# Kernel optimization log

Hardware: AMD Instinct MI355X
Metric: run time of the kernel (lower is better)

## Reference

```python
import jax, jax.numpy as jnp
import numpy as np
from jax import lax

BIG = 1e10  # initial distance, matching torch's 1e10


def farthest_point_sample(xyz, init_farthest, npoint):
    """xyz: [B,N,3] float; init_farthest: [B] int32; returns centroids [B,npoint] int32."""
    B, N, _ = xyz.shape
    batch_idx = jnp.arange(B)

    def body(i, state):
        centroids, distance, farthest = state
        centroids = centroids.at[:, i].set(farthest)
        c = xyz[batch_idx, farthest][:, None, :]              # [B,1,3] current centroid
        dist = jnp.sum(jnp.square(xyz - c), axis=-1)          # [B,N] sq. distance
        distance = jnp.minimum(distance, dist)                # mask-update: keep min dist to any centroid
        farthest = jnp.argmax(distance, axis=-1).astype(jnp.int32)
        return centroids, distance, farthest

    centroids0 = jnp.zeros((B, npoint), jnp.int32)
    distance0 = jnp.full((B, N), BIG, xyz.dtype)
    centroids, _, _ = lax.fori_loop(0, npoint, body, (centroids0, distance0, init_farthest.astype(jnp.int32)))
    return centroids


def setup_inputs() -> dict:
    key = jax.random.key(0)
    k1, k2, k3 = jax.random.split(key, 3)
    B, N = 16, 100000
    mesh = jax.random.normal(k1, (B, N, 3), dtype=jnp.float32)
    contact_map = jax.random.uniform(k2, (B, N, 1), dtype=jnp.float32)
    init_farthest = jax.random.randint(k3, (B,), 0, N, dtype=jnp.int32)
    return {"mesh": mesh, "contact_map": contact_map, "init_farthest": init_farthest, "npoint": 1024}


def reference(mesh, contact_map, init_farthest, npoint):
    B, N, _ = mesh.shape
    batch_idx = jnp.arange(B)

    # __compute_mesh_scale: max distance from centroid, per batch
    centroid = jnp.mean(mesh, axis=1, keepdims=True)                      # [B,1,3]
    s_obj = jnp.max(jnp.sqrt(jnp.sum(jnp.square(mesh - centroid), axis=2)), axis=1)  # [B]

    # __farthest_point_sample
    centroids = farthest_point_sample(mesh, init_farthest, npoint)        # [B,npoint]

    # gather sampled points and contact values
    point_cloud = mesh[batch_idx[:, None], centroids]                     # [B,npoint,3]
    cm_sampled = contact_map[batch_idx[:, None], centroids]               # [B,npoint,1]

    # normalize by object scale (broadcast over points/coords)
    point_cloud_norm = point_cloud / s_obj[:, None, None]

    # point_cloud_norm_contact fed to the contact encoder in the original
    return jnp.concatenate([cm_sampled, point_cloud_norm], axis=2)        # [B,npoint,4]
```

## Files before the change

kernel.cpp:

```cpp
#include <hip/hip_runtime.h>
#include <cstdint>

#define NBATCH 16
#define NPOINT 1024
#define NPTS   100000
#define GPB    16
#define TPB    256
#define WPB    4
#define NSUB   16
#define STRIDE (GPB * TPB)
#define KPT    25
#define NPAIR  13

typedef unsigned long long u64;
typedef unsigned int u32;


__global__ __launch_bounds__(256) void sum_kernel(const float* __restrict__ xyz,
                                                  float* __restrict__ psum) {
    const int b   = blockIdx.x & 15;
    const int sub = blockIdx.x >> 4;
    const float* P = xyz + (size_t)b * NPTS * 3;
    float sx = 0.f, sy = 0.f, sz = 0.f;
    for (int i = sub * TPB + threadIdx.x; i < NPTS; i += NSUB * TPB) {
        sx += P[i * 3 + 0];
        sy += P[i * 3 + 1];
        sz += P[i * 3 + 2];
    }
    #pragma unroll
    for (int off = 32; off; off >>= 1) {
        sx += __shfl_xor(sx, off);
        sy += __shfl_xor(sy, off);
        sz += __shfl_xor(sz, off);
    }
    __shared__ float r[3][4];
    const int wave = threadIdx.x >> 6, lane = threadIdx.x & 63;
    if (lane == 0) { r[0][wave] = sx; r[1][wave] = sy; r[2][wave] = sz; }
    __syncthreads();
    if (threadIdx.x == 0) {
        float* o = psum + (b * NSUB + sub) * 4;
        o[0] = r[0][0] + r[0][1] + r[0][2] + r[0][3];
        o[1] = r[1][0] + r[1][1] + r[1][2] + r[1][3];
        o[2] = r[2][0] + r[2][1] + r[2][2] + r[2][3];
    }
}

__global__ __launch_bounds__(256) void max_kernel(const float* __restrict__ xyz,
                                                  const float* __restrict__ psum,
                                                  unsigned* __restrict__ pmax,
                                                  u64* __restrict__ slots) {
    if (blockIdx.x == 0) {
        slots[threadIdx.x] = 0ull;
        slots[threadIdx.x + 256] = 0ull;
    }
    const int b   = blockIdx.x & 15;
    const int sub = blockIdx.x >> 4;
    const float* P = xyz + (size_t)b * NPTS * 3;
    float sx = 0.f, sy = 0.f, sz = 0.f;
    #pragma unroll
    for (int s = 0; s < NSUB; ++s) {
        sx += psum[(b * NSUB + s) * 4 + 0];
        sy += psum[(b * NSUB + s) * 4 + 1];
        sz += psum[(b * NSUB + s) * 4 + 2];
    }
    const float mx = sx / (float)NPTS, my = sy / (float)NPTS, mz = sz / (float)NPTS;
    float best = 0.f;
    for (int i = sub * TPB + threadIdx.x; i < NPTS; i += NSUB * TPB) {
        float dx = P[i * 3 + 0] - mx;
        float dy = P[i * 3 + 1] - my;
        float dz = P[i * 3 + 2] - mz;
        best = fmaxf(best, dx * dx + dy * dy + dz * dz);
    }
    #pragma unroll
    for (int off = 32; off; off >>= 1) best = fmaxf(best, __shfl_xor(best, off));
    __shared__ float r[4];
    const int wave = threadIdx.x >> 6, lane = threadIdx.x & 63;
    if (lane == 0) r[wave] = best;
    __syncthreads();
    if (threadIdx.x == 0)
        pmax[b * NSUB + sub] = __float_as_uint(fmaxf(fmaxf(r[0], r[1]), fmaxf(r[2], r[3])));
}

__device__ __forceinline__ u64 wave_max_u64(u64 k) {
    u32 lo = (u32)k, hi = (u32)(k >> 32);
    #define DPP_STEP(CTRL) do {                                                          \
        u32 olo = (u32)__builtin_amdgcn_update_dpp((int)lo, (int)lo, CTRL, 0xf, 0xf, false); \
        u32 ohi = (u32)__builtin_amdgcn_update_dpp((int)hi, (int)hi, CTRL, 0xf, 0xf, false); \
        u64 oo = ((u64)ohi << 32) | olo;                                                 \
        u64 cc = ((u64)hi  << 32) | lo;                                                  \
        if (oo > cc) { lo = olo; hi = ohi; }                                             \
    } while (0)
    DPP_STEP(0x111);
    DPP_STEP(0x112);
    DPP_STEP(0x114);
    DPP_STEP(0x118);
    DPP_STEP(0x142);
    DPP_STEP(0x143);
    #undef DPP_STEP
    return ((u64)hi << 32) | lo;
}

__device__ __forceinline__ u64 bcast_lane63(u64 v) {
    u32 lo = (u32)__builtin_amdgcn_readlane((int)(u32)v, 63);
    u32 hi = (u32)__builtin_amdgcn_readlane((int)(u32)(v >> 32), 63);
    return ((u64)hi << 32) | lo;
}

__device__ __forceinline__ void store_agent(u64* p, u64 v) {
    __hip_atomic_store(p, v, __ATOMIC_RELAXED, __HIP_MEMORY_SCOPE_AGENT);
}
__device__ __forceinline__ u64 load_agent(u64* p) {
    return __hip_atomic_load(p, __ATOMIC_RELAXED, __HIP_MEMORY_SCOPE_AGENT);
}

__global__ void
__attribute__((amdgpu_flat_work_group_size(256, 256), amdgpu_waves_per_eu(1, 1)))
fps_kernel(const float* __restrict__ xyz,
           const float* __restrict__ cmap,
           const int* __restrict__ init_far,
           const unsigned* __restrict__ pmax,
           u64* __restrict__ slots,
           float* __restrict__ out) {
    const int b   = blockIdx.x & 15;
    const int g   = blockIdx.x >> 4;
    const int tid = threadIdx.x;
    const int wave = tid >> 6, lane = tid & 63;
    const int tl  = g * TPB + tid;
    const float* P = xyz + (size_t)b * NPTS * 3;

    float m0 = 0.f;
    #pragma unroll
    for (int s = 0; s < NSUB; ++s) m0 = fmaxf(m0, __uint_as_float(pmax[b * NSUB + s]));
    const float sb = sqrtf(m0);

    float pxx[NPAIR], pxy[NPAIR], pyx[NPAIR], pyy[NPAIR],
          pzx[NPAIR], pzy[NPAIR], pdx[NPAIR], pdy[NPAIR];
    #pragma unroll
    for (int j = 0; j < NPAIR; ++j) {
        const int p0 = tl + (2 * j) * STRIDE;
        const int p1 = tl + (2 * j + 1) * STRIDE;
        const bool v0 = p0 < NPTS, v1 = p1 < NPTS;
        pxx[j] = v0 ? P[p0 * 3 + 0] : 0.f;  pxy[j] = v1 ? P[p1 * 3 + 0] : 0.f;
        pyx[j] = v0 ? P[p0 * 3 + 1] : 0.f;  pyy[j] = v1 ? P[p1 * 3 + 1] : 0.f;
        pzx[j] = v0 ? P[p0 * 3 + 2] : 0.f;  pzy[j] = v1 ? P[p1 * 3 + 2] : 0.f;
        pdx[j] = v0 ? 1e10f : -1.0f;        pdy[j] = v1 ? 1e10f : -1.0f;
    }

    __shared__ u64 lkey[WPB];
    __shared__ u64 pub;
    __shared__ int curhist[NPOINT];
    if (tid == 0) pub = 0;
    if (tid < WPB) lkey[tid] = 0;
    __syncthreads();

    int cur = init_far[b];
    float cx = P[cur * 3 + 0], cy = P[cur * 3 + 1], cz = P[cur * 3 + 2];

    for (int i = 0; i < NPOINT; ++i) {
        if (tid == 192) curhist[i] = cur;
        if (i == NPOINT - 1) break;

        float best = -1.0f;
        int bidx = 0;
        {
            #pragma clang fp contract(off)
            #pragma unroll
            for (int j = 0; j < NPAIR; ++j) {
                float dx0 = pxx[j] - cx, dx1 = pxy[j] - cx;
                float dy0 = pyx[j] - cy, dy1 = pyy[j] - cy;
                float dz0 = pzx[j] - cz, dz1 = pzy[j] - cz;
                float s0 = dx0 * dx0 + dy0 * dy0;  float s1 = dx1 * dx1 + dy1 * dy1;
                s0 = s0 + dz0 * dz0;               s1 = s1 + dz1 * dz1;
                float n0 = fminf(pdx[j], s0);      float n1 = fminf(pdy[j], s1);
                pdx[j] = n0;                       pdy[j] = n1;
                if (n0 > best) { best = n0; bidx = tl + (2 * j) * STRIDE; }
                if (n1 > best) { best = n1; bidx = tl + (2 * j + 1) * STRIDE; }
            }
        }

        const u64 want = (u64)(i + 1);
        u64 key = ((u64)__float_as_uint(best) << 22) | (u64)(0x3FFFFFu - (unsigned)bidx);
        const u64 wkey = wave_max_u64(key) | (want << 54);
        if (lane == 63)
            __hip_atomic_store(&lkey[wave], wkey, __ATOMIC_RELAXED,
                               __HIP_MEMORY_SCOPE_WORKGROUP);

        u64* const bs = slots + ((size_t)(i & 1) * NBATCH + b) * GPB;

        if (wave == 0) {
            u64 k;
            for (;;) {
                k = (lane < WPB)
                    ? __hip_atomic_load(&lkey[lane], __ATOMIC_RELAXED,
                                        __HIP_MEMORY_SCOPE_WORKGROUP)
                    : (want << 54);
                if (__all((int)((k >> 54) >= want))) break;
            }
            const u64 bk = wave_max_u64(lane < WPB ? k : 0);
            if (lane == 63) store_agent(&bs[g], bk);

            u64 v;
            {
                u64* sp = &bs[lane & 15];
                u64 vcur = load_agent(sp);
                u64 vnxt = load_agent(sp);
                int tries = 0;
                for (;;) {
                    if (__all((int)((vcur >> 54) >= want))) { v = vcur; break; }
                    vcur = vnxt;
                    vnxt = load_agent(sp);
                    if (++tries > 64) __builtin_amdgcn_s_sleep(1);
                }
            }

            const u64 w = bcast_lane63(wave_max_u64(v));
            if (lane == 0)
                __hip_atomic_store(&pub, w, __ATOMIC_RELAXED,
                                   __HIP_MEMORY_SCOPE_WORKGROUP);
            cur = (int)(0x3FFFFFu - (unsigned)(w & 0x3FFFFFu));
        } else {
            u64 pv;
            int tries = 0;
            for (;;) {
                pv = __hip_atomic_load(&pub, __ATOMIC_RELAXED,
                                       __HIP_MEMORY_SCOPE_WORKGROUP);
                if ((pv >> 54) >= want) break;
                if (++tries > 64) __builtin_amdgcn_s_sleep(1);
            }
            cur = (int)(0x3FFFFFu - (unsigned)(pv & 0x3FFFFFu));
        }

        cx = P[cur * 3 + 0];
        cy = P[cur * 3 + 1];
        cz = P[cur * 3 + 2];
    }

    __syncthreads();
    if (tid < 64) {
        const int row = g * 64 + tid;
        const int c   = curhist[row];
        const float cm = cmap[(size_t)b * NPTS + c];
        const float x = P[c * 3 + 0], y = P[c * 3 + 1], z = P[c * 3 + 2];
        float* o = out + ((size_t)b * NPOINT + row) * 4;
        o[0] = cm;
        o[1] = x / sb;
        o[2] = y / sb;
        o[3] = z / sb;
    }
}

extern "C" void kernel_launch(void* const* d_in, const int* in_sizes, int n_in,
                              void* d_out, int out_size, void* d_ws, size_t ws_size,
                              hipStream_t stream) {
    const float* mesh = (const float*)d_in[0];
    const float* cmap = (const float*)d_in[1];
    const int* init   = (const int*)d_in[2];
    float* out = (float*)d_out;

    char* ws      = (char*)d_ws;
    float* psum   = (float*)ws;
    unsigned* pmx = (unsigned*)(ws + 4096);
    u64* slots    = (u64*)(ws + 8192);

    sum_kernel<<<dim3(256), dim3(TPB), 0, stream>>>(mesh, psum);
    max_kernel<<<dim3(256), dim3(TPB), 0, stream>>>(mesh, psum, pmx, slots);
    fps_kernel<<<dim3(256), dim3(TPB), 0, stream>>>(mesh, cmap, init, pmx, slots, out);
}
```

Measured before the change: 1.970 ms.

## Use leader-block reduction with single result slot for cross-block argmax sync

Instead of every block polling all 16 per-batch collection slots each iteration, only block g==0 gathers the 16 partial maxima, reduces them, and publishes one result word. The other blocks poll that single result slot. This cuts redundant global-memory polling traffic and contention on the collection slots. The cost is an extra serial hop through the leader block, which adds latency to every iteration of the farthest-point loop.

```diff
diff --git a/kernel.cpp b/kernel.cpp
--- a/kernel.cpp
+++ b/kernel.cpp
@@ -50,8 +50,8 @@
                                                   unsigned* __restrict__ pmax,
                                                   u64* __restrict__ slots) {
     if (blockIdx.x == 0) {
-        slots[threadIdx.x] = 0ull;
-        slots[threadIdx.x + 256] = 0ull;
+        #pragma unroll
+        for (int k = 0; k < 4; ++k) slots[threadIdx.x + 256 * k] = 0ull;
     }
     const int b   = blockIdx.x & 15;
     const int sub = blockIdx.x >> 4;
@@ -119,7 +119,8 @@
            const float* __restrict__ cmap,
            const int* __restrict__ init_far,
            const unsigned* __restrict__ pmax,
-           u64* __restrict__ slots,
+           u64* __restrict__ coll,
+           u64* __restrict__ res,
            float* __restrict__ out) {
     const int b   = blockIdx.x & 15;
     const int g   = blockIdx.x >> 4;
@@ -185,7 +186,8 @@
             __hip_atomic_store(&lkey[wave], wkey, __ATOMIC_RELAXED,
                                __HIP_MEMORY_SCOPE_WORKGROUP);
 
-        u64* const bs = slots + ((size_t)(i & 1) * NBATCH + b) * GPB;
+        u64* const cl = coll + ((size_t)(i & 1) * NBATCH + b) * GPB;
+        u64* const rl = res  + ((size_t)(i & 1) * NBATCH + b) * GPB;
 
         if (wave == 0) {
             u64 k;
@@ -197,23 +199,37 @@
                 if (__all((int)((k >> 54) >= want))) break;
             }
             const u64 bk = wave_max_u64(lane < WPB ? k : 0);
-            if (lane == 63) store_agent(&bs[g], bk);
-
-            u64 v;
-            {
-                u64* sp = &bs[lane & 15];
-                u64 vcur = load_agent(sp);
-                u64 vnxt = load_agent(sp);
+            if (lane == 63) store_agent(&cl[g], bk);
+
+            u64 w;
+            if (g == 0) {
+                u64 v;
+                {
+                    u64* sp = &cl[lane & 15];
+                    u64 vcur = load_agent(sp);
+                    u64 vnxt = load_agent(sp);
+                    int tries = 0;
+                    for (;;) {
+                        if (__all((int)((vcur >> 54) >= want))) { v = vcur; break; }
+                        vcur = vnxt;
+                        vnxt = load_agent(sp);
+                        if (++tries > 64) __builtin_amdgcn_s_sleep(1);
+                    }
+                }
+                w = bcast_lane63(wave_max_u64(v));
+                if (lane == 0) store_agent(&rl[0], w);
+            } else {
+                u64 vcur = load_agent(&rl[0]);
+                u64 vnxt = load_agent(&rl[0]);
                 int tries = 0;
                 for (;;) {
-                    if (__all((int)((vcur >> 54) >= want))) { v = vcur; break; }
+                    if (__all((int)((vcur >> 54) >= want))) { w = vcur; break; }
                     vcur = vnxt;
-                    vnxt = load_agent(sp);
+                    vnxt = load_agent(&rl[0]);
                     if (++tries > 64) __builtin_amdgcn_s_sleep(1);
                 }
             }
 
-            const u64 w = bcast_lane63(wave_max_u64(v));
             if (lane == 0)
                 __hip_atomic_store(&pub, w, __ATOMIC_RELAXED,
                                    __HIP_MEMORY_SCOPE_WORKGROUP);
@@ -261,8 +277,10 @@
     float* psum   = (float*)ws;
     unsigned* pmx = (unsigned*)(ws + 4096);
     u64* slots    = (u64*)(ws + 8192);
+    u64* coll     = (u64*)(ws + 8192);
+    u64* res      = (u64*)(ws + 12288);
 
     sum_kernel<<<dim3(256), dim3(TPB), 0, stream>>>(mesh, psum);
     max_kernel<<<dim3(256), dim3(TPB), 0, stream>>>(mesh, psum, pmx, slots);
-    fps_kernel<<<dim3(256), dim3(TPB), 0, stream>>>(mesh, cmap, init, pmx, slots, out);
-}
+    fps_kernel<<<dim3(256), dim3(TPB), 0, stream>>>(mesh, cmap, init, pmx, coll, res, out);
+}
```

New measurement: 2.732 ms. +38.7%, slower.

## Carry winning point coordinates through reductions instead of reloading from global memory

Applied to the files above, without the earlier changes.

The argmax reductions at wave, block and grid level now carry the candidate point's xyz alongside the key, via DPP and versioned slots. The next centroid's coordinates arrive with the winning index, so the dependent global load of P[cur] at the end of each serial iteration is gone. In exchange, every reduction step moves five words instead of two, the cross-block slots grow fourfold, and more LDS and agent-scope stores are needed per iteration.

```diff
diff --git a/kernel.cpp b/kernel.cpp
--- a/kernel.cpp
+++ b/kernel.cpp
@@ -50,8 +50,8 @@
                                                   unsigned* __restrict__ pmax,
                                                   u64* __restrict__ slots) {
     if (blockIdx.x == 0) {
-        slots[threadIdx.x] = 0ull;
-        slots[threadIdx.x + 256] = 0ull;
+        #pragma unroll
+        for (int k = 0; k < 8; ++k) slots[threadIdx.x + 256 * k] = 0ull;
     }
     const int b   = blockIdx.x & 15;
     const int sub = blockIdx.x >> 4;
@@ -90,12 +90,8 @@
         u64 cc = ((u64)hi  << 32) | lo;                                                  \
         if (oo > cc) { lo = olo; hi = ohi; }                                             \
     } while (0)
-    DPP_STEP(0x111);
-    DPP_STEP(0x112);
-    DPP_STEP(0x114);
-    DPP_STEP(0x118);
-    DPP_STEP(0x142);
-    DPP_STEP(0x143);
+    DPP_STEP(0x111); DPP_STEP(0x112); DPP_STEP(0x114);
+    DPP_STEP(0x118); DPP_STEP(0x142); DPP_STEP(0x143);
     #undef DPP_STEP
     return ((u64)hi << 32) | lo;
 }
@@ -106,11 +102,28 @@
     return ((u64)hi << 32) | lo;
 }
 
+#define TSTEP(CTRL) do {                                                                   \
+    u32 oklo = (u32)__builtin_amdgcn_update_dpp((int)klo, (int)klo, CTRL, 0xf, 0xf, false); \
+    u32 okhi = (u32)__builtin_amdgcn_update_dpp((int)khi, (int)khi, CTRL, 0xf, 0xf, false); \
+    u32 ox   = (u32)__builtin_amdgcn_update_dpp((int)tx,  (int)tx,  CTRL, 0xf, 0xf, false); \
+    u32 oy   = (u32)__builtin_amdgcn_update_dpp((int)ty,  (int)ty,  CTRL, 0xf, 0xf, false); \
+    u32 oz   = (u32)__builtin_amdgcn_update_dpp((int)tz,  (int)tz,  CTRL, 0xf, 0xf, false); \
+    u64 oo = ((u64)okhi << 32) | oklo;                                                     \
+    u64 cc = ((u64)khi  << 32) | klo;                                                      \
+    if (oo > cc) { klo = oklo; khi = okhi; tx = ox; ty = oy; tz = oz; }                    \
+} while (0)
+
 __device__ __forceinline__ void store_agent(u64* p, u64 v) {
     __hip_atomic_store(p, v, __ATOMIC_RELAXED, __HIP_MEMORY_SCOPE_AGENT);
 }
 __device__ __forceinline__ u64 load_agent(u64* p) {
     return __hip_atomic_load(p, __ATOMIC_RELAXED, __HIP_MEMORY_SCOPE_AGENT);
+}
+__device__ __forceinline__ void st_lds(u64* p, u64 v) {
+    __hip_atomic_store(p, v, __ATOMIC_RELAXED, __HIP_MEMORY_SCOPE_WORKGROUP);
+}
+__device__ __forceinline__ u64 ld_lds(u64* p) {
+    return __hip_atomic_load(p, __ATOMIC_RELAXED, __HIP_MEMORY_SCOPE_WORKGROUP);
 }
 
 __global__ void
@@ -146,11 +159,11 @@
         pdx[j] = v0 ? 1e10f : -1.0f;        pdy[j] = v1 ? 1e10f : -1.0f;
     }
 
-    __shared__ u64 lkey[WPB];
-    __shared__ u64 pub;
+    __shared__ u64 lkw[WPB * 4];
+    __shared__ u64 pubw[4];
     __shared__ int curhist[NPOINT];
-    if (tid == 0) pub = 0;
-    if (tid < WPB) lkey[tid] = 0;
+    if (tid < WPB * 4) lkw[tid] = 0;
+    if (tid == 64) { pubw[0] = 0; pubw[1] = 0; pubw[2] = 0; pubw[3] = 0; }
     __syncthreads();
 
     int cur = init_far[b];
@@ -162,6 +175,7 @@
 
         float best = -1.0f;
         int bidx = 0;
+        float bx = 0.f, by = 0.f, bz = 0.f;
         {
             #pragma clang fp contract(off)
             #pragma unroll
@@ -173,35 +187,63 @@
                 s0 = s0 + dz0 * dz0;               s1 = s1 + dz1 * dz1;
                 float n0 = fminf(pdx[j], s0);      float n1 = fminf(pdy[j], s1);
                 pdx[j] = n0;                       pdy[j] = n1;
-                if (n0 > best) { best = n0; bidx = tl + (2 * j) * STRIDE; }
-                if (n1 > best) { best = n1; bidx = tl + (2 * j + 1) * STRIDE; }
+                if (n0 > best) { best = n0; bidx = tl + (2 * j) * STRIDE;
+                                 bx = pxx[j]; by = pyx[j]; bz = pzx[j]; }
+                if (n1 > best) { best = n1; bidx = tl + (2 * j + 1) * STRIDE;
+                                 bx = pxy[j]; by = pyy[j]; bz = pzy[j]; }
             }
         }
 
         const u64 want = (u64)(i + 1);
-        u64 key = ((u64)__float_as_uint(best) << 22) | (u64)(0x3FFFFFu - (unsigned)bidx);
-        const u64 wkey = wave_max_u64(key) | (want << 54);
-        if (lane == 63)
-            __hip_atomic_store(&lkey[wave], wkey, __ATOMIC_RELAXED,
-                               __HIP_MEMORY_SCOPE_WORKGROUP);
-
-        u64* const bs = slots + ((size_t)(i & 1) * NBATCH + b) * GPB;
+        const u64 key = (want << 54) | ((u64)__float_as_uint(best) << 22)
+                                     | (u64)(0x3FFFFFu - (unsigned)bidx);
+        u32 klo = (u32)key, khi = (u32)(key >> 32);
+        u32 tx = __float_as_uint(bx), ty = __float_as_uint(by), tz = __float_as_uint(bz);
+        TSTEP(0x111); TSTEP(0x112); TSTEP(0x114);
+        TSTEP(0x118); TSTEP(0x142); TSTEP(0x143);
+        if (lane == 63) {
+            st_lds(&lkw[wave * 4 + 0], ((u64)khi << 32) | klo);
+            st_lds(&lkw[wave * 4 + 1], (want << 54) | tx);
+            st_lds(&lkw[wave * 4 + 2], (want << 54) | ty);
+            st_lds(&lkw[wave * 4 + 3], (want << 54) | tz);
+        }
+
+        u64* const bs = slots + ((size_t)(i & 1) * NBATCH + b) * (GPB * 4);
 
         if (wave == 0) {
-            u64 k;
             for (;;) {
-                k = (lane < WPB)
-                    ? __hip_atomic_load(&lkey[lane], __ATOMIC_RELAXED,
-                                        __HIP_MEMORY_SCOPE_WORKGROUP)
-                    : (want << 54);
-                if (__all((int)((k >> 54) >= want))) break;
-            }
-            const u64 bk = wave_max_u64(lane < WPB ? k : 0);
-            if (lane == 63) store_agent(&bs[g], bk);
+                u64 m = (lane < WPB * 4) ? ld_lds(&lkw[lane]) : (want << 54);
+                if (__all((int)((m >> 54) >= want))) break;
+            }
+            {
+                const int wv = lane & 3;
+                u64 k  = ld_lds(&lkw[wv * 4 + 0]);
+                u64 xw = ld_lds(&lkw[wv * 4 + 1]);
+                u64 yw = ld_lds(&lkw[wv * 4 + 2]);
+                u64 zw = ld_lds(&lkw[wv * 4 + 3]);
+                u32 klo2 = (u32)k, khi2 = (u32)(k >> 32);
+                u32 tx2 = (u32)xw, ty2 = (u32)yw, tz2 = (u32)zw;
+                {
+                    u32 klo = klo2, khi = khi2, tx = tx2, ty = ty2, tz = tz2;
+                    TSTEP(0x111); TSTEP(0x112);
+                    klo2 = klo; khi2 = khi; tx2 = tx; ty2 = ty; tz2 = tz;
+                }
+                const u32 bklo = (u32)__builtin_amdgcn_readlane((int)klo2, 3);
+                const u32 bkhi = (u32)__builtin_amdgcn_readlane((int)khi2, 3);
+                const u32 bbx  = (u32)__builtin_amdgcn_readlane((int)tx2, 3);
+                const u32 bby  = (u32)__builtin_amdgcn_readlane((int)ty2, 3);
+                const u32 bbz  = (u32)__builtin_amdgcn_readlane((int)tz2, 3);
+                if (lane == 0) {
+                    store_agent(&bs[g * 4 + 0], ((u64)bkhi << 32) | bklo);
+                    store_agent(&bs[g * 4 + 1], (want << 54) | bbx);
+                    store_agent(&bs[g * 4 + 2], (want << 54) | bby);
+                    store_agent(&bs[g * 4 + 3], (want << 54) | bbz);
+                }
+            }
 
             u64 v;
             {
-                u64* sp = &bs[lane & 15];
+                u64* sp = &bs[((lane & 15) << 2) | (lane >> 4)];
                 u64 vcur = load_agent(sp);
                 u64 vnxt = load_agent(sp);
                 int tries = 0;
@@ -213,26 +255,36 @@
                 }
             }
 
-            const u64 w = bcast_lane63(wave_max_u64(v));
-            if (lane == 0)
-                __hip_atomic_store(&pub, w, __ATOMIC_RELAXED,
-                                   __HIP_MEMORY_SCOPE_WORKGROUP);
-            cur = (int)(0x3FFFFFu - (unsigned)(w & 0x3FFFFFu));
+            const u64 wkey = bcast_lane63(wave_max_u64(lane < 16 ? v : 0));
+            const u32 idxw = 0x3FFFFFu - (u32)(wkey & 0x3FFFFFu);
+            const int gs   = (int)((idxw & (STRIDE - 1)) >> 8);
+            const u32 xb = (u32)__builtin_amdgcn_readlane((int)(u32)v, 16 + gs);
+            const u32 yb = (u32)__builtin_amdgcn_readlane((int)(u32)v, 32 + gs);
+            const u32 zb = (u32)__builtin_amdgcn_readlane((int)(u32)v, 48 + gs);
+
+            if (lane == 0) {
+                st_lds(&pubw[1], (want << 54) | xb);
+                st_lds(&pubw[2], (want << 54) | yb);
+                st_lds(&pubw[3], (want << 54) | zb);
+                st_lds(&pubw[0], wkey);
+            }
+            cur = (int)idxw;
+            cx = __uint_as_float(xb); cy = __uint_as_float(yb); cz = __uint_as_float(zb);
         } else {
             u64 pv;
             int tries = 0;
             for (;;) {
-                pv = __hip_atomic_load(&pub, __ATOMIC_RELAXED,
-                                       __HIP_MEMORY_SCOPE_WORKGROUP);
-                if ((pv >> 54) >= want) break;
+                pv = ld_lds(&pubw[lane & 3]);
+                if (__all((int)((pv >> 54) >= want))) break;
                 if (++tries > 64) __builtin_amdgcn_s_sleep(1);
             }
-            cur = (int)(0x3FFFFFu - (unsigned)(pv & 0x3FFFFFu));
+            const u32 w0lo = (u32)__builtin_amdgcn_readlane((int)(u32)pv, 0);
+            const u32 xb   = (u32)__builtin_amdgcn_readlane((int)(u32)pv, 1);
+            const u32 yb   = (u32)__builtin_amdgcn_readlane((int)(u32)pv, 2);
+            const u32 zb   = (u32)__builtin_amdgcn_readlane((int)(u32)pv, 3);
+            cur = (int)(0x3FFFFFu - (w0lo & 0x3FFFFFu));
+            cx = __uint_as_float(xb); cy = __uint_as_float(yb); cz = __uint_as_float(zb);
         }
-
-        cx = P[cur * 3 + 0];
-        cy = P[cur * 3 + 1];
-        cz = P[cur * 3 + 2];
     }
 
     __syncthreads();
```

Measured after the change: 4.663 ms. +136.7%, slower.
